# Performance work log

Hardware: AMD Instinct MI355X
Metric: run time of the kernel (lower is better)

Reference implementation:

```python
import jax, jax.numpy as jnp
import numpy as np

B, N, DIM, H, DH, MLP, L = 4, 1024, 1024, 16, 64, 4096, 2
C = DIM // 4  # conditioning dim = 256


def setup_inputs() -> dict:
    key = jax.random.key(0)
    ks = jax.random.split(key, 12)
    s = 0.02
    return dict(
        x=jax.random.normal(ks[0], (B, N, DIM), jnp.float32),
        mu=jax.random.normal(ks[1], (B, N, C), jnp.float32),
        f=jax.random.normal(ks[2], (B, N, C), jnp.float32),
        Wqkv=jax.random.normal(ks[3], (L, DIM, 3 * H * DH), jnp.float32) * s,
        Wout=jax.random.normal(ks[4], (L, H * DH, DIM), jnp.float32) * s,
        bout=jnp.zeros((L, DIM), jnp.float32),
        W1=jax.random.normal(ks[5], (L, DIM, MLP), jnp.float32) * s,
        b1=jnp.zeros((L, MLP), jnp.float32),
        W2=jax.random.normal(ks[6], (L, MLP, DIM), jnp.float32) * s,
        b2=jnp.zeros((L, DIM), jnp.float32),
        Wmu=jax.random.normal(ks[7], (L, C, 6 * C), jnp.float32) * s,
        bmu=jnp.zeros((L, 6 * C), jnp.float32),
        Wf=jax.random.normal(ks[8], (L, C, 6 * 3 * C), jnp.float32) * s,
        bf=jnp.zeros((L, 6 * 3 * C), jnp.float32),
        g1=jnp.ones((L, DIM), jnp.float32),
        be1=jnp.zeros((L, DIM), jnp.float32),
        g2=jnp.ones((L, DIM), jnp.float32),
        be2=jnp.zeros((L, DIM), jnp.float32),
    )


def _ln(x, g, b):
    m = jnp.mean(x, -1, keepdims=True)
    v = jnp.mean((x - m) ** 2, -1, keepdims=True)
    return (x - m) * jax.lax.rsqrt(v + 1e-5) * g + b


def reference(x, mu, f, Wqkv, Wout, bout, W1, b1, W2, b2, Wmu, bmu, Wf, bf, g1, be1, g2, be2):
    scale = DH ** -0.5
    smu = jax.nn.silu(mu)  # SiLU applied to raw conditioning, shared across layers
    sf = jax.nn.silu(f)
    for i in range(L):
        mm = smu @ Wmu[i] + bmu[i]          # [B,N,6*C]
        mf = sf @ Wf[i] + bf[i]             # [B,N,6*3*C]
        mus = jnp.split(mm, 6, axis=-1)     # each [B,N,C]
        fs = jnp.split(mf, 6, axis=-1)      # each [B,N,3C]
        sh_a, sc_a, ga_a, sh_m, sc_m, ga_m = [
            jnp.concatenate([a, b_], -1) for a, b_ in zip(mus, fs)
        ]                                   # each [B,N,DIM]
        # attention branch
        h = _ln(x, g1[i], be1[i]) * (1 + sc_a) + sh_a
        qkv = h @ Wqkv[i]                   # [B,N,3*H*DH]
        q, k, v = [t.reshape(B, N, H, DH) for t in jnp.split(qkv, 3, axis=-1)]
        att = jax.nn.softmax(jnp.einsum('bihd,bjhd->bhij', q, k) * scale, axis=-1)
        o = jnp.einsum('bhij,bjhd->bihd', att, v).reshape(B, N, H * DH)
        x = x + ga_a * (o @ Wout[i] + bout[i])
        # MLP branch
        h2 = _ln(x, g2[i], be2[i]) * (1 + sc_m) + sh_m
        mlp = jax.nn.gelu(h2 @ W1[i] + b1[i], approximate=False) @ W2[i] + b2[i]
        x = x + ga_m * mlp
    return x
```

## Files before the change

### kernel.cpp

```cpp
#include <hip/hip_runtime.h>
#include <math.h>

#define BB 4
#define NN 1024
#define DIMD 1024
#define HHN 16
#define DHH 64
#define MLPD 4096
#define LLN 2
#define CCD 256
#define BNROWS (BB*NN)

typedef __attribute__((ext_vector_type(8))) _Float16 h8;
typedef __attribute__((ext_vector_type(4))) _Float16 h4;
typedef __attribute__((ext_vector_type(4))) float f32x4;

#define GLD16(gp, lp) __builtin_amdgcn_global_load_lds( \
    (const __attribute__((address_space(1))) void*)(gp), \
    (__attribute__((address_space(3))) void*)(lp), 16, 0, 0)

__global__ __launch_bounds__(256) void silu_kernel(const float* __restrict__ in,
                                                   _Float16* __restrict__ out, int n4) {
  int i = blockIdx.x * 256 + threadIdx.x;
  if (i < n4) {
    float4 v = ((const float4*)in)[i];
    h4 o;
    o[0] = (_Float16)(v.x / (1.f + __expf(-v.x)));
    o[1] = (_Float16)(v.y / (1.f + __expf(-v.y)));
    o[2] = (_Float16)(v.z / (1.f + __expf(-v.z)));
    o[3] = (_Float16)(v.w / (1.f + __expf(-v.w)));
    ((h4*)out)[i] = o;
  }
}

__global__ __launch_bounds__(256) void transpose_cast(const float* __restrict__ in,
                                                      _Float16* __restrict__ out,
                                                      int K, int N) {
  __shared__ float tile[64][68];
  int bx = blockIdx.x * 64;
  int by = blockIdx.y * 64;
  int tid = threadIdx.x;
  int r0 = tid >> 4, c4 = (tid & 15) * 4;
  #pragma unroll
  for (int i = 0; i < 4; i++) {
    float4 v = *(const float4*)(in + (size_t)(by + r0 + i * 16) * N + bx + c4);
    *(float4*)&tile[r0 + i * 16][c4] = v;
  }
  __syncthreads();
  #pragma unroll
  for (int i = 0; i < 4; i++) {
    int orow = r0 + i * 16;
    h4 o;
    #pragma unroll
    for (int j = 0; j < 4; j++) o[j] = (_Float16)tile[c4 + j][orow];
    *(h4*)(out + (size_t)(bx + orow) * K + by + c4) = o;
  }
}

__global__ __launch_bounds__(256) void v_transpose(const _Float16* __restrict__ qkv,
                                                   _Float16* __restrict__ vt) {
  __shared__ _Float16 t[64][72];
  int n0 = blockIdx.x * 64;
  int bh = blockIdx.y;
  int b = bh >> 4;
  const _Float16* src = qkv + (size_t)b * NN * 3072 + 2048 + (bh & 15) * 64;
  int tid = threadIdx.x;
  int row = tid >> 2, c0 = (tid & 3) * 16;
  *(h8*)&t[row][c0] = *(const h8*)(src + (size_t)(n0 + row) * 3072 + c0);
  *(h8*)&t[row][c0 + 8] = *(const h8*)(src + (size_t)(n0 + row) * 3072 + c0 + 8);
  __syncthreads();
  int d = tid >> 2, ns = (tid & 3) * 16;
  h8 o0, o1;
  #pragma unroll
  for (int j = 0; j < 8; j++) { o0[j] = t[ns + j][d]; o1[j] = t[ns + 8 + j][d]; }
  _Float16* dst = vt + ((size_t)bh * 64 + d) * NN + n0 + ns;
  *(h8*)dst = o0;
  *(h8*)(dst + 8) = o1;
}

template <int EPI, int BNT>
__global__ __launch_bounds__(256) void gemm_bt(
    const _Float16* __restrict__ A, const _Float16* __restrict__ Bt,
    int M, int Nt, int K,
    const float* __restrict__ bias,
    _Float16* __restrict__ outh,
    float* __restrict__ xio,
    const _Float16* __restrict__ mmb, const _Float16* __restrict__ mfb, int gchunk) {
  constexpr int NREP = BNT / 32;
  __shared__ _Float16 As[2][128 * 32];
  __shared__ _Float16 Bs[2][BNT * 32];
  const int tid = threadIdx.x;
  const int wave = tid >> 6, lane = tid & 63;
  const int brow = blockIdx.x * 128, bcol = blockIdx.y * BNT;
  const int wr = (wave >> 1) * 64, wc = (wave & 1) * (BNT / 2);
  const int r = lane & 15, g = lane >> 4;
  f32x4 acc[4][NREP];
  #pragma unroll
  for (int m = 0; m < 4; m++)
    #pragma unroll
    for (int n = 0; n < NREP; n++) acc[m][n] = (f32x4){0.f, 0.f, 0.f, 0.f};

  const _Float16* gA = A + (size_t)(brow + wave * 32 + (lane >> 2)) * K + (lane & 3) * 8;
  const _Float16* gB = Bt + (size_t)(bcol + wave * (BNT / 4) + (lane >> 2)) * K + (lane & 3) * 8;

  auto STAGE = [&](int b, int k0) {
    GLD16(gA + k0, &As[b][wave * 1024]);
    GLD16(gA + k0 + 16 * (size_t)K, &As[b][wave * 1024 + 512]);
    if (BNT == 128) {
      GLD16(gB + k0, &Bs[b][wave * 1024]);
      GLD16(gB + k0 + 16 * (size_t)K, &Bs[b][wave * 1024 + 512]);
    } else {
      GLD16(gB + k0, &Bs[b][wave * 512]);
    }
  };

  STAGE(0, 0);
  int cur = 0;
  for (int k0 = 0; k0 < K; k0 += 32) {
    __syncthreads();
    if (k0 + 32 < K) STAGE(cur ^ 1, k0 + 32);
    h8 af[4], bfr[NREP];
    #pragma unroll
    for (int m = 0; m < 4; m++) af[m] = *(const h8*)(&As[cur][(wr + m * 16 + r) * 32 + g * 8]);
    #pragma unroll
    for (int n = 0; n < NREP; n++) bfr[n] = *(const h8*)(&Bs[cur][(wc + n * 16 + r) * 32 + g * 8]);
    #pragma unroll
    for (int m = 0; m < 4; m++)
      #pragma unroll
      for (int n = 0; n < NREP; n++)
        acc[m][n] = __builtin_amdgcn_mfma_f32_16x16x32_f16(bfr[n], af[m], acc[m][n], 0, 0, 0);
    cur ^= 1;
  }

  #pragma unroll
  for (int m = 0; m < 4; m++) {
    const int grow = brow + wr + m * 16 + r;
    #pragma unroll
    for (int n = 0; n < NREP; n++) {
      const int gcol = bcol + wc + n * 16 + 4 * g;
      float4 bv4 = bias ? *(const float4*)(bias + gcol) : float4{0.f, 0.f, 0.f, 0.f};
      float v[4] = {acc[m][n][0] + bv4.x, acc[m][n][1] + bv4.y,
                    acc[m][n][2] + bv4.z, acc[m][n][3] + bv4.w};
      if (EPI == 0) {
        h4 o;
        #pragma unroll
        for (int q = 0; q < 4; q++) o[q] = (_Float16)v[q];
        *(h4*)(outh + (size_t)grow * Nt + gcol) = o;
      } else if (EPI == 1) {
        h4 o;
        #pragma unroll
        for (int q = 0; q < 4; q++)
          o[q] = (_Float16)(0.5f * v[q] * (1.f + erff(v[q] * 0.70710678118f)));
        *(h4*)(outh + (size_t)grow * Nt + gcol) = o;
      } else {
        h4 gav = (gcol < CCD)
            ? *(const h4*)(mmb + (size_t)grow * (6 * CCD) + gchunk * CCD + gcol)
            : *(const h4*)(mfb + (size_t)grow * (18 * CCD) + gchunk * (3 * CCD) + (gcol - CCD));
        float4 xv = *(float4*)(xio + (size_t)grow * DIMD + gcol);
        xv.x += (float)gav[0] * v[0];
        xv.y += (float)gav[1] * v[1];
        xv.z += (float)gav[2] * v[2];
        xv.w += (float)gav[3] * v[3];
        *(float4*)(xio + (size_t)grow * DIMD + gcol) = xv;
      }
    }
  }
}

__global__ __launch_bounds__(256) void ln_mod(const float* __restrict__ x,
                                              const float* __restrict__ gam,
                                              const float* __restrict__ bet,
                                              const _Float16* __restrict__ mmb,
                                              const _Float16* __restrict__ mfb,
                                              int jsh, int jsc,
                                              _Float16* __restrict__ hout) {
  const int row = blockIdx.x;
  const int tid = threadIdx.x;
  const float* xr = x + (size_t)row * DIMD;
  float4 v = ((const float4*)xr)[tid];
  float s = v.x + v.y + v.z + v.w;
  float sq = v.x * v.x + v.y * v.y + v.z * v.z + v.w * v.w;
  #pragma unroll
  for (int off = 32; off > 0; off >>= 1) {
    s += __shfl_down(s, off);
    sq += __shfl_down(sq, off);
  }
  __shared__ float red[8];
  int wv = tid >> 6, ln = tid & 63;
  if (ln == 0) { red[wv] = s; red[4 + wv] = sq; }
  __syncthreads();
  s = red[0] + red[1] + red[2] + red[3];
  sq = red[4] + red[5] + red[6] + red[7];
  float mean = s * (1.f / DIMD);
  float var = sq * (1.f / DIMD) - mean * mean;
  float rs = rsqrtf(var + 1e-5f);
  int c0 = tid * 4;
  float4 gm = ((const float4*)gam)[tid];
  float4 bt = ((const float4*)bet)[tid];
  float xv[4] = {v.x, v.y, v.z, v.w};
  float gv[4] = {gm.x, gm.y, gm.z, gm.w};
  float bv[4] = {bt.x, bt.y, bt.z, bt.w};
  h4 o;
  #pragma unroll
  for (int i = 0; i < 4; i++) {
    int c = c0 + i;
    float lnv = (xv[i] - mean) * rs * gv[i] + bv[i];
    float shv, scv;
    if (c < CCD) {
      shv = (float)mmb[(size_t)row * (6 * CCD) + jsh * CCD + c];
      scv = (float)mmb[(size_t)row * (6 * CCD) + jsc * CCD + c];
    } else {
      shv = (float)mfb[(size_t)row * (18 * CCD) + jsh * (3 * CCD) + (c - CCD)];
      scv = (float)mfb[(size_t)row * (18 * CCD) + jsc * (3 * CCD) + (c - CCD)];
    }
    o[i] = (_Float16)(lnv * (1.f + scv) + shv);
  }
  *((h4*)(hout + (size_t)row * DIMD + c0)) = o;
}

__global__ __launch_bounds__(256) void attn_kernel(const _Float16* __restrict__ qkv,
                                                   const _Float16* __restrict__ vt,
                                                   _Float16* __restrict__ o) {
  __shared__ _Float16 Ks[2 * 64 * 64];
  __shared__ _Float16 Vs[2 * 64 * 64];
  __shared__ _Float16 Ps[4][32 * 72];
  const int bhg = blockIdx.x * 8 + (blockIdx.y & 7);
  const int qt = blockIdx.y >> 3;
  const int b = bhg >> 4, hh = bhg & 15;
  const int tid = threadIdx.x;
  const int wave = tid >> 6, lane = tid & 63;
  const int r = lane & 15, g = lane >> 4;
  const int RS = 3 * HHN * DHH;
  const _Float16* qb = qkv + (size_t)b * NN * RS + hh * DHH;
  const _Float16* kb = qb + HHN * DHH;
  const _Float16* vtb = vt + (size_t)bhg * DHH * NN;
  const int q0 = qt * 128 + wave * 32;

  h8 qf[2][2];
  #pragma unroll
  for (int m = 0; m < 2; m++) {
    qf[m][0] = *(const h8*)(qb + (size_t)(q0 + m * 16 + r) * RS + g * 8);
    qf[m][1] = *(const h8*)(qb + (size_t)(q0 + m * 16 + r) * RS + 32 + g * 8);
  }

  f32x4 oacc[2][4];
  #pragma unroll
  for (int m = 0; m < 2; m++)
    #pragma unroll
    for (int n = 0; n < 4; n++) oacc[m][n] = (f32x4){0.f, 0.f, 0.f, 0.f};
  float mrun[2][4], lrun[2][4];
  #pragma unroll
  for (int m = 0; m < 2; m++)
    #pragma unroll
    for (int q = 0; q < 4; q++) { mrun[m][q] = -1e30f; lrun[m][q] = 0.f; }
  const float scale = 0.125f;
  _Float16* Pw = Ps[wave];

  auto STAGE = [&](int buf, int k0) {
    #pragma unroll
    for (int i = 0; i < 2; i++) {
      int chunk = wave * 2 + i;
      int blk = chunk * 64 + lane;
      int row = blk >> 3, c16 = blk & 7;
      int sc = ((c16 ^ (row & 7))) * 8;
      GLD16(kb + (size_t)(k0 + row) * RS + sc, Ks + buf * 4096 + chunk * 512);
      GLD16(vtb + (size_t)row * NN + k0 + sc, Vs + buf * 4096 + chunk * 512);
    }
  };

  STAGE(0, 0);
  int cur = 0;
  for (int kt = 0; kt < NN / 64; ++kt) {
    __syncthreads();
    if (kt + 1 < NN / 64) STAGE(cur ^ 1, (kt + 1) * 64);
    const _Float16* Kb = Ks + cur * 4096;
    const _Float16* Vb = Vs + cur * 4096;
    f32x4 sfr[2][4];
    #pragma unroll
    for (int m = 0; m < 2; m++)
      #pragma unroll
      for (int n = 0; n < 4; n++) sfr[m][n] = (f32x4){0.f, 0.f, 0.f, 0.f};
    #pragma unroll
    for (int n = 0; n < 4; n++) {
      int row = n * 16 + r, sw = row & 7;
      h8 kf0 = *(const h8*)(Kb + row * 64 + (g ^ sw) * 8);
      h8 kf1 = *(const h8*)(Kb + row * 64 + ((4 + g) ^ sw) * 8);
      #pragma unroll
      for (int m = 0; m < 2; m++) {
        sfr[m][n] = __builtin_amdgcn_mfma_f32_16x16x32_f16(qf[m][0], kf0, sfr[m][n], 0, 0, 0);
        sfr[m][n] = __builtin_amdgcn_mfma_f32_16x16x32_f16(qf[m][1], kf1, sfr[m][n], 0, 0, 0);
      }
    }
    #pragma unroll
    for (int m = 0; m < 2; m++) {
      float pm[4];
      #pragma unroll
      for (int q = 0; q < 4; q++)
        pm[q] = fmaxf(fmaxf(sfr[m][0][q], sfr[m][1][q]), fmaxf(sfr[m][2][q], sfr[m][3][q])) * scale;
      #pragma unroll
      for (int off = 1; off < 16; off <<= 1)
        #pragma unroll
        for (int q = 0; q < 4; q++) pm[q] = fmaxf(pm[q], __shfl_xor(pm[q], off));
      float fac[4], rsum[4];
      #pragma unroll
      for (int q = 0; q < 4; q++) {
        float mn = fmaxf(mrun[m][q], pm[q]);
        fac[q] = __expf(mrun[m][q] - mn);
        mrun[m][q] = mn;
        rsum[q] = 0.f;
      }
      #pragma unroll
      for (int n = 0; n < 4; n++)
        #pragma unroll
        for (int q = 0; q < 4; q++) {
          float p = __expf(sfr[m][n][q] * scale - mrun[m][q]);
          sfr[m][n][q] = p;
          rsum[q] += p;
        }
      #pragma unroll
      for (int off = 1; off < 16; off <<= 1)
        #pragma unroll
        for (int q = 0; q < 4; q++) rsum[q] += __shfl_xor(rsum[q], off);
      #pragma unroll
      for (int q = 0; q < 4; q++) lrun[m][q] = lrun[m][q] * fac[q] + rsum[q];
      #pragma unroll
      for (int n = 0; n < 4; n++)
        #pragma unroll
        for (int q = 0; q < 4; q++) oacc[m][n][q] *= fac[q];
      #pragma unroll
      for (int n = 0; n < 4; n++)
        #pragma unroll
        for (int q = 0; q < 4; q++)
          Pw[(m * 16 + 4 * g + q) * 72 + n * 16 + r] = (_Float16)sfr[m][n][q];
    }
    h8 pa[2][2];
    #pragma unroll
    for (int m = 0; m < 2; m++) {
      pa[m][0] = *(const h8*)(Pw + (m * 16 + r) * 72 + g * 8);
      pa[m][1] = *(const h8*)(Pw + (m * 16 + r) * 72 + 32 + g * 8);
    }
    #pragma unroll
    for (int nd = 0; nd < 4; nd++) {
      int row = nd * 16 + r, sw = row & 7;
      h8 vf0 = *(const h8*)(Vb + row * 64 + (g ^ sw) * 8);
      h8 vf1 = *(const h8*)(Vb + row * 64 + ((4 + g) ^ sw) * 8);
      #pragma unroll
      for (int m = 0; m < 2; m++) {
        oacc[m][nd] = __builtin_amdgcn_mfma_f32_16x16x32_f16(pa[m][0], vf0, oacc[m][nd], 0, 0, 0);
        oacc[m][nd] = __builtin_amdgcn_mfma_f32_16x16x32_f16(pa[m][1], vf1, oacc[m][nd], 0, 0, 0);
      }
    }
    cur ^= 1;
  }
  #pragma unroll
  for (int m = 0; m < 2; m++)
    #pragma unroll
    for (int nd = 0; nd < 4; nd++)
      #pragma unroll
      for (int q = 0; q < 4; q++) {
        int row = q0 + m * 16 + 4 * g + q;
        int col = hh * DHH + nd * 16 + r;
        o[((size_t)b * NN + row) * DIMD + col] = (_Float16)(oacc[m][nd][q] / lrun[m][q]);
      }
}

extern "C" void kernel_launch(void* const* d_in, const int* in_sizes, int n_in,
                              void* d_out, int out_size, void* d_ws, size_t ws_size,
                              hipStream_t stream) {
  (void)in_sizes; (void)n_in; (void)out_size; (void)ws_size;
  const float* mu   = (const float*)d_in[1];
  const float* f_in = (const float*)d_in[2];
  const float* Wqkv = (const float*)d_in[3];
  const float* Wout = (const float*)d_in[4];
  const float* bout = (const float*)d_in[5];
  const float* W1   = (const float*)d_in[6];
  const float* b1   = (const float*)d_in[7];
  const float* W2   = (const float*)d_in[8];
  const float* b2   = (const float*)d_in[9];
  const float* Wmu  = (const float*)d_in[10];
  const float* bmu  = (const float*)d_in[11];
  const float* Wf   = (const float*)d_in[12];
  const float* bfv  = (const float*)d_in[13];
  const float* g1   = (const float*)d_in[14];
  const float* be1  = (const float*)d_in[15];
  const float* g2   = (const float*)d_in[16];
  const float* be2  = (const float*)d_in[17];
  float* xout = (float*)d_out;

  char* ws = (char*)d_ws;
  size_t off = 0;
  auto alloc = [&](size_t elems) -> _Float16* {
    _Float16* p = (_Float16*)(ws + off);
    off += ((elems * 2 + 255) / 256) * 256;
    return p;
  };
  _Float16* wTqkv = alloc((size_t)LLN * 3072 * 1024);
  _Float16* wTout = alloc((size_t)LLN * 1024 * 1024);
  _Float16* wT1   = alloc((size_t)LLN * 4096 * 1024);
  _Float16* wT2   = alloc((size_t)LLN * 1024 * 4096);
  _Float16* wTmu  = alloc((size_t)LLN * 1536 * 256);
  _Float16* wTf   = alloc((size_t)LLN * 4608 * 256);
  _Float16* smu   = alloc((size_t)BNROWS * CCD);
  _Float16* sfb   = alloc((size_t)BNROWS * CCD);
  _Float16* mmb   = alloc((size_t)BNROWS * 6 * CCD);
  _Float16* mfb   = alloc((size_t)BNROWS * 18 * CCD);
  _Float16* hbuf  = alloc((size_t)BNROWS * DIMD);
  _Float16* qkvb  = alloc((size_t)BNROWS * 3 * DIMD);
  _Float16* obuf  = alloc((size_t)BNROWS * DIMD);
  _Float16* m1b   = alloc((size_t)BNROWS * MLPD);
  _Float16* vtb   = alloc((size_t)BNROWS * DIMD);

  hipMemcpyAsync(d_out, d_in[0], (size_t)BNROWS * DIMD * sizeof(float),
                 hipMemcpyDeviceToDevice, stream);

  silu_kernel<<<BNROWS * CCD / 4 / 256, 256, 0, stream>>>(mu, smu, BNROWS * CCD / 4);
  silu_kernel<<<BNROWS * CCD / 4 / 256, 256, 0, stream>>>(f_in, sfb, BNROWS * CCD / 4);

  for (int l = 0; l < LLN; l++) {
    transpose_cast<<<dim3(3072 / 64, 1024 / 64), 256, 0, stream>>>(
        Wqkv + (size_t)l * 1024 * 3072, wTqkv + (size_t)l * 3072 * 1024, 1024, 3072);
    transpose_cast<<<dim3(1024 / 64, 1024 / 64), 256, 0, stream>>>(
        Wout + (size_t)l * 1024 * 1024, wTout + (size_t)l * 1024 * 1024, 1024, 1024);
    transpose_cast<<<dim3(4096 / 64, 1024 / 64), 256, 0, stream>>>(
        W1 + (size_t)l * 1024 * 4096, wT1 + (size_t)l * 4096 * 1024, 1024, 4096);
    transpose_cast<<<dim3(1024 / 64, 4096 / 64), 256, 0, stream>>>(
        W2 + (size_t)l * 4096 * 1024, wT2 + (size_t)l * 1024 * 4096, 4096, 1024);
    transpose_cast<<<dim3(1536 / 64, 256 / 64), 256, 0, stream>>>(
        Wmu + (size_t)l * 256 * 1536, wTmu + (size_t)l * 1536 * 256, 256, 1536);
    transpose_cast<<<dim3(4608 / 64, 256 / 64), 256, 0, stream>>>(
        Wf + (size_t)l * 256 * 4608, wTf + (size_t)l * 4608 * 256, 256, 4608);
  }

  for (int l = 0; l < LLN; l++) {
    gemm_bt<0, 64><<<dim3(BNROWS / 128, 1536 / 64), 256, 0, stream>>>(
        smu, wTmu + (size_t)l * 1536 * 256, BNROWS, 1536, 256,
        bmu + (size_t)l * 1536, mmb, nullptr, nullptr, nullptr, 0);
    gemm_bt<0, 128><<<dim3(BNROWS / 128, 4608 / 128), 256, 0, stream>>>(
        sfb, wTf + (size_t)l * 4608 * 256, BNROWS, 4608, 256,
        bfv + (size_t)l * 4608, mfb, nullptr, nullptr, nullptr, 0);
    ln_mod<<<BNROWS, 256, 0, stream>>>(xout, g1 + (size_t)l * DIMD, be1 + (size_t)l * DIMD,
                                       mmb, mfb, 0, 1, hbuf);
    gemm_bt<0, 128><<<dim3(BNROWS / 128, 3072 / 128), 256, 0, stream>>>(
        hbuf, wTqkv + (size_t)l * 3072 * 1024, BNROWS, 3072, 1024,
        nullptr, qkvb, nullptr, nullptr, nullptr, 0);
    v_transpose<<<dim3(NN / 64, BB * HHN), 256, 0, stream>>>(qkvb, vtb);
    attn_kernel<<<dim3(NN / 128, BB * HHN), 256, 0, stream>>>(qkvb, vtb, obuf);
    gemm_bt<2, 64><<<dim3(BNROWS / 128, 1024 / 64), 256, 0, stream>>>(
        obuf, wTout + (size_t)l * 1024 * 1024, BNROWS, 1024, 1024,
        bout + (size_t)l * DIMD, nullptr, xout, mmb, mfb, 2);
    ln_mod<<<BNROWS, 256, 0, stream>>>(xout, g2 + (size_t)l * DIMD, be2 + (size_t)l * DIMD,
                                       mmb, mfb, 3, 4, hbuf);
    gemm_bt<1, 128><<<dim3(BNROWS / 128, 4096 / 128), 256, 0, stream>>>(
        hbuf, wT1 + (size_t)l * 4096 * 1024, BNROWS, 4096, 1024,
        b1 + (size_t)l * MLPD, m1b, nullptr, nullptr, nullptr, 0);
    gemm_bt<2, 64><<<dim3(BNROWS / 128, 1024 / 64), 256, 0, stream>>>(
        m1b, wT2 + (size_t)l * 1024 * 4096, BNROWS, 1024, 4096,
        b2 + (size_t)l * DIMD, nullptr, xout, mmb, mfb, 5);
  }
}
```

Before: 710.7 us.

## Triple-buffer GEMM LDS staging with explicit vmcnt waits

```diff
diff --git a/kernel.cpp b/kernel.cpp
--- a/kernel.cpp
+++ b/kernel.cpp
@@ -87,8 +87,8 @@
     float* __restrict__ xio,
     const _Float16* __restrict__ mmb, const _Float16* __restrict__ mfb, int gchunk) {
   constexpr int NREP = BNT / 32;
-  __shared__ _Float16 As[2][128 * 32];
-  __shared__ _Float16 Bs[2][BNT * 32];
+  __shared__ _Float16 As[3][128 * 32];
+  __shared__ _Float16 Bs[3][BNT * 32];
   const int tid = threadIdx.x;
   const int wave = tid >> 6, lane = tid & 63;
   const int brow = blockIdx.x * 128, bcol = blockIdx.y * BNT;
@@ -103,22 +103,35 @@
   const _Float16* gA = A + (size_t)(brow + wave * 32 + (lane >> 2)) * K + (lane & 3) * 8;
   const _Float16* gB = Bt + (size_t)(bcol + wave * (BNT / 4) + (lane >> 2)) * K + (lane & 3) * 8;
 
-  auto STAGE = [&](int b, int k0) {
-    GLD16(gA + k0, &As[b][wave * 1024]);
-    GLD16(gA + k0 + 16 * (size_t)K, &As[b][wave * 1024 + 512]);
+  auto STAGE = [&](int slot, int k0) {
+    GLD16(gA + k0, &As[slot][wave * 1024]);
+    GLD16(gA + k0 + 16 * (size_t)K, &As[slot][wave * 1024 + 512]);
     if (BNT == 128) {
-      GLD16(gB + k0, &Bs[b][wave * 1024]);
-      GLD16(gB + k0 + 16 * (size_t)K, &Bs[b][wave * 1024 + 512]);
+      GLD16(gB + k0, &Bs[slot][wave * 1024]);
+      GLD16(gB + k0 + 16 * (size_t)K, &Bs[slot][wave * 1024 + 512]);
     } else {
-      GLD16(gB + k0, &Bs[b][wave * 512]);
+      GLD16(gB + k0, &Bs[slot][wave * 512]);
     }
   };
 
-  STAGE(0, 0);
+  const int NT = K / 32;
+  #pragma unroll
+  for (int s = 0; s < 3; ++s)
+    if (s < NT) STAGE(s, s * 32);
+
   int cur = 0;
-  for (int k0 = 0; k0 < K; k0 += 32) {
-    __syncthreads();
-    if (k0 + 32 < K) STAGE(cur ^ 1, k0 + 32);
+  for (int t = 0; t < NT; ++t) {
+    const int rem = NT - 1 - t;
+    if constexpr (BNT == 128) {
+      if (rem >= 2)      asm volatile("s_waitcnt vmcnt(8)" ::: "memory");
+      else if (rem == 1) asm volatile("s_waitcnt vmcnt(4)" ::: "memory");
+      else               asm volatile("s_waitcnt vmcnt(0)" ::: "memory");
+    } else {
+      if (rem >= 2)      asm volatile("s_waitcnt vmcnt(6)" ::: "memory");
+      else if (rem == 1) asm volatile("s_waitcnt vmcnt(3)" ::: "memory");
+      else               asm volatile("s_waitcnt vmcnt(0)" ::: "memory");
+    }
+    __builtin_amdgcn_s_barrier();
     h8 af[4], bfr[NREP];
     #pragma unroll
     for (int m = 0; m < 4; m++) af[m] = *(const h8*)(&As[cur][(wr + m * 16 + r) * 32 + g * 8]);
@@ -129,7 +142,10 @@
       #pragma unroll
       for (int n = 0; n < NREP; n++)
         acc[m][n] = __builtin_amdgcn_mfma_f32_16x16x32_f16(bfr[n], af[m], acc[m][n], 0, 0, 0);
-    cur ^= 1;
+    asm volatile("s_waitcnt lgkmcnt(0)" ::: "memory");
+    __builtin_amdgcn_s_barrier();
+    if (t + 3 < NT) STAGE(cur, (t + 3) * 32);
+    cur = (cur == 2) ? 0 : cur + 1;
   }
 
   #pragma unroll
```

New measurement: 711.6 us. About the same (+0.1%).
